# Optimization experiments

Measured on AMD Instinct MI355X. Metric: run time of the kernel, lower is better.

Reference implementation:

```python
import jax, jax.numpy as jnp
import numpy as np

N = 16384
IN_DIM = 11
D = 64
L = 4
K = 16 + 1  # self.k + 1 (n >= k+1)
EPS = 1e-5


def _bn(x, g, b):
    # BatchNorm1d in training mode: biased batch stats over the edge/node axis
    m = jnp.mean(x, axis=0)
    v = jnp.var(x, axis=0)
    return g * (x - m) * jax.lax.rsqrt(v + EPS) + b


def _mlp(x, W1, b1, g1, be1, W2, b2, g2, be2):
    x = jax.nn.relu(_bn(x @ W1 + b1, g1, be1))
    x = jax.nn.relu(_bn(x @ W2 + b2, g2, be2))
    return x


def _knn_edges(h):
    # torch.cdist + topk(-d, K); row 0 of idx.T is the (self) nearest node
    hs = jax.lax.stop_gradient(h)  # only indices are used downstream
    sq = jnp.sum(hs * hs, axis=-1)
    d2 = sq[:, None] + sq[None, :] - 2.0 * (hs @ hs.T)  # (n, n)
    d = jnp.sqrt(jnp.maximum(d2, 0.0))
    _, idx = jax.lax.top_k(-d, K)  # (n, K)
    frm = jnp.tile(idx[:, 0], K - 1)            # from_nodes = row0 repeated
    to = idx[:, 1:].T.reshape(-1)               # to_nodes = rows 1..K-1 flattened
    return frm, to


def setup_inputs() -> dict:
    key = jax.random.key(0)
    ks = jax.random.split(key, 8)
    s = 0.05
    inp = {
        "pos": jax.random.normal(ks[0], (N, IN_DIM), jnp.float32),
        "lin_in_W": jax.random.normal(ks[1], (IN_DIM, D), jnp.float32) * s,
        "lin_in_b": jnp.zeros((D,), jnp.float32),
        "pred_W": jax.random.normal(ks[2], (D, 1), jnp.float32) * s,
        "pred_b": jnp.zeros((1,), jnp.float32),
    }
    i = 3
    for pre in ("msg", "upd"):
        inp[f"{pre}_W1"] = jax.random.normal(ks[i], (L, 2 * D, D), jnp.float32) * s
        inp[f"{pre}_b1"] = jnp.zeros((L, D), jnp.float32)
        inp[f"{pre}_g1"] = jnp.ones((L, D), jnp.float32)
        inp[f"{pre}_be1"] = jnp.zeros((L, D), jnp.float32)
        inp[f"{pre}_W2"] = jax.random.normal(ks[i + 1], (L, D, D), jnp.float32) * s
        inp[f"{pre}_b2"] = jnp.zeros((L, D), jnp.float32)
        inp[f"{pre}_g2"] = jnp.ones((L, D), jnp.float32)
        inp[f"{pre}_be2"] = jnp.zeros((L, D), jnp.float32)
        i += 2
    return inp


def reference(pos, lin_in_W, lin_in_b, pred_W, pred_b,
              msg_W1, msg_b1, msg_g1, msg_be1, msg_W2, msg_b2, msg_g2, msg_be2,
              upd_W1, upd_b1, upd_g1, upd_be1, upd_W2, upd_b2, upd_g2, upd_be2):
    h = pos @ lin_in_W + lin_in_b  # (n, d)
    for l in range(L):
        frm, to = _knn_edges(h)
        # PyG source_to_target: h_j = h[edge_index[0]] (source), h_i = h[edge_index[1]] (dest)
        h_i = h[to]
        h_j = h[frm]
        msg = _mlp(jnp.concatenate([h_i, h_j], axis=-1),
                   msg_W1[l], msg_b1[l], msg_g1[l], msg_be1[l],
                   msg_W2[l], msg_b2[l], msg_g2[l], msg_be2[l])  # (e, d)
        agg = jax.ops.segment_sum(msg, to, num_segments=N)  # scatter-add at dest
        upd = _mlp(jnp.concatenate([h, agg], axis=-1),
                   upd_W1[l], upd_b1[l], upd_g1[l], upd_be1[l],
                   upd_W2[l], upd_b2[l], upd_g2[l], upd_be2[l])
        h = h + upd  # residual
    h_graph = jnp.mean(h, axis=0, keepdims=True)  # global_mean_pool, single graph
    out = h_graph @ pred_W + pred_b
    return out.reshape(-1)
```

## Files before the change

### kernel.cpp

```cpp
#include <hip/hip_runtime.h>

#define NN 16384
#define KP1 17
#define EE (NN*16)
#define CAP 448

typedef short bf16x8 __attribute__((ext_vector_type(8)));
typedef float f32x16 __attribute__((ext_vector_type(16)));

__device__ __forceinline__ ushort f2bf(float f) {
  unsigned u = __float_as_uint(f);
  unsigned r = (u + 0x7fffu + ((u >> 16) & 1u)) >> 16;
  return (ushort)r;
}
__device__ __forceinline__ float bf2f(ushort s) { return __uint_as_float(((unsigned)s) << 16); }

__global__ __launch_bounds__(256) void k_lin_in(const float* __restrict__ pos,
    const float* __restrict__ W, const float* __restrict__ b, float* __restrict__ h) {
  const int t = blockIdx.x*256 + threadIdx.x;
  const int n = t >> 6, c = t & 63;
  float acc = b[c];
  #pragma unroll
  for (int k = 0; k < 11; ++k) acc = fmaf(pos[n*11+k], W[k*64+c], acc);
  h[t] = acc;
}

__global__ __launch_bounds__(256) void k_prep_all(const float* __restrict__ h, float* __restrict__ sq,
    ushort* __restrict__ pk, ushort* __restrict__ hbh, ushort* __restrict__ hbl) {
  const int row = blockIdx.x*256 + threadIdx.x;
  const int tile = row >> 5, rl = row & 31;
  const float4* rp = (const float4*)(h + (size_t)row*64);
  float s = 0.f;
  #pragma unroll
  for (int q = 0; q < 16; ++q) {
    const float4 x = rp[q];
    s += x.x*x.x + x.y*x.y + x.z*x.z + x.w*x.w;
    ushort4 hi, lo;
    hi.x = f2bf(x.x); lo.x = f2bf(x.x - bf2f(hi.x));
    hi.y = f2bf(x.y); lo.y = f2bf(x.y - bf2f(hi.y));
    hi.z = f2bf(x.z); lo.z = f2bf(x.z - bf2f(hi.z));
    hi.w = f2bf(x.w); lo.w = f2bf(x.w - bf2f(hi.w));
    *(ushort4*)(hbh + (size_t)row*64 + q*4) = hi;
    *(ushort4*)(hbl + (size_t)row*64 + q*4) = lo;
    const int ks = q >> 2, sub = (q >> 1) & 1, e = (q & 1)*4;
    const int lane = rl + 32*sub;
    ushort* base = pk + (size_t)tile*4096 + ks*1024 + (size_t)lane*8 + e;
    *(ushort4*)(base)       = hi;
    *(ushort4*)(base + 512) = lo;
  }
  sq[row] = s;
}

__global__ __launch_bounds__(256) void k_wprep(const float* __restrict__ W1all,
    const float* __restrict__ W2all, ushort* __restrict__ wp1, ushort* __restrict__ wp2) {
  const int t = blockIdx.x*256 + threadIdx.x;
  if (t < 4096) {
    const int lane = t & 63, ks = (t>>6)&7, mt = (t>>9)&1, l = t>>10;
    const int m = mt*32 + (lane&31);
    const int k0 = ks*16 + (lane>>5)*8;
    const float* w = W1all + l*8192;
    ushort* dst = wp1 + ((((size_t)l*2 + mt)*8 + ks)*2)*512 + (size_t)lane*8;
    #pragma unroll
    for (int e = 0; e < 8; ++e) {
      const float v = w[(k0+e)*64 + m];
      const ushort hi = f2bf(v);
      dst[e] = hi; dst[512+e] = f2bf(v - bf2f(hi));
    }
  } else if (t < 6144) {
    const int t2 = t - 4096;
    const int lane = t2 & 63, ks = (t2>>6)&3, mt = (t2>>8)&1, l = t2>>9;
    const int m = mt*32 + (lane&31);
    const int k0 = ks*16 + (lane>>5)*8;
    const float* w = W2all + l*4096;
    ushort* dst = wp2 + ((((size_t)l*2 + mt)*4 + ks)*2)*512 + (size_t)lane*8;
    #pragma unroll
    for (int e = 0; e < 8; ++e) {
      const float v = w[(k0+e)*64 + m];
      const ushort hi = f2bf(v);
      dst[e] = hi; dst[512+e] = f2bf(v - bf2f(hi));
    }
  }
}

struct F8 { bf16x8 h0,h1,h2,h3,l0,l1,l2,l3; };

__device__ __forceinline__ void ldf(const ushort* __restrict__ pk, int tile, int lane, F8& f) {
  const ushort* tp = pk + (size_t)tile*4096 + (size_t)lane*8;
  f.h0 = *(const bf16x8*)(tp);
  f.l0 = *(const bf16x8*)(tp + 512);
  f.h1 = *(const bf16x8*)(tp + 1024);
  f.l1 = *(const bf16x8*)(tp + 1536);
  f.h2 = *(const bf16x8*)(tp + 2048);
  f.l2 = *(const bf16x8*)(tp + 2560);
  f.h3 = *(const bf16x8*)(tp + 3072);
  f.l3 = *(const bf16x8*)(tp + 3584);
}

#define MF(A,B,C) __builtin_amdgcn_mfma_f32_32x32x16_bf16(A,B,C,0,0,0)

__device__ __forceinline__ void tile_keys2(const F8& fa, const F8& fb,
    const bf16x8 (&bqh)[4], const bf16x8 (&bql)[4], const float* __restrict__ sq,
    const int ta, const int tb, const int lhi, float (&ka)[16], float (&kb)[16]) {
  f32x16 a, b;
  #pragma unroll
  for (int i = 0; i < 16; ++i) { a[i] = 0.f; b[i] = 0.f; }
  a = MF(fa.h0, bqh[0], a);  b = MF(fb.h0, bqh[0], b);
  a = MF(fa.h0, bql[0], a);  b = MF(fb.h0, bql[0], b);
  a = MF(fa.l0, bqh[0], a);  b = MF(fb.l0, bqh[0], b);
  a = MF(fa.h1, bqh[1], a);  b = MF(fb.h1, bqh[1], b);
  a = MF(fa.h1, bql[1], a);  b = MF(fb.h1, bql[1], b);
  a = MF(fa.l1, bqh[1], a);  b = MF(fb.l1, bqh[1], b);
  a = MF(fa.h2, bqh[2], a);  b = MF(fb.h2, bqh[2], b);
  a = MF(fa.h2, bql[2], a);  b = MF(fb.h2, bql[2], b);
  a = MF(fa.l2, bqh[2], a);  b = MF(fb.l2, bqh[2], b);
  a = MF(fa.h3, bqh[3], a);  b = MF(fb.h3, bqh[3], b);
  a = MF(fa.h3, bql[3], a);  b = MF(fb.h3, bql[3], b);
  a = MF(fa.l3, bqh[3], a);  b = MF(fb.l3, bqh[3], b);
  const int c0a = ta*32, c0b = tb*32;
  #pragma unroll
  for (int g = 0; g < 4; ++g) {
    const float4 va = *(const float4*)(sq + c0a + g*8 + 4*lhi);
    const float4 vb = *(const float4*)(sq + c0b + g*8 + 4*lhi);
    ka[g*4+0] = fmaf(-2.f, a[g*4+0], va.x);
    ka[g*4+1] = fmaf(-2.f, a[g*4+1], va.y);
    ka[g*4+2] = fmaf(-2.f, a[g*4+2], va.z);
    ka[g*4+3] = fmaf(-2.f, a[g*4+3], va.w);
    kb[g*4+0] = fmaf(-2.f, b[g*4+0], vb.x);
    kb[g*4+1] = fmaf(-2.f, b[g*4+1], vb.y);
    kb[g*4+2] = fmaf(-2.f, b[g*4+2], vb.z);
    kb[g*4+3] = fmaf(-2.f, b[g*4+3], vb.w);
  }
}

#define HIST1(K) { _Pragma("unroll") for (int r = 0; r < 16; ++r) { \
    unsigned x = __float_as_uint(K[r]); x = (x & 0x80000000u) ? ~x : (x | 0x80000000u); \
    atomicAdd(&hist[x >> 24][qcol], 1u); } }
#define HIST2(K) { _Pragma("unroll") for (int r = 0; r < 16; ++r) { \
    unsigned x = __float_as_uint(K[r]); x = (x & 0x80000000u) ? ~x : (x | 0x80000000u); \
    if ((x >> 24) == b1) atomicAdd(&hist[(x >> 16) & 255u][qcol], 1u); } }
#define COLLECT(K, TILE) { _Pragma("unroll") for (int r = 0; r < 16; ++r) { \
    if (K[r] <= bfq) { \
      unsigned x = __float_as_uint(K[r]); x = (x & 0x80000000u) ? ~x : (x | 0x80000000u); \
      const unsigned slot = atomicAdd(&ccnt[qcol], 1u); \
      if (slot < CAP) { \
        const int cidx = (TILE)*32 + (r & 3) + 8*(r >> 2) + 4*lhi; \
        coll[(size_t)q*CAP + slot] = ((unsigned long long)x << 32) | (unsigned)cidx; } } } }

__global__ __launch_bounds__(512) void k_knn(const ushort* __restrict__ pk,
    const float* __restrict__ sq, unsigned long long* __restrict__ coll,
    unsigned* __restrict__ gcnt) {
  __shared__ unsigned hist[256][32];
  __shared__ unsigned part[16][32];
  __shared__ unsigned bin1s[32], below1s[32];
  __shared__ float boundf[32];
  __shared__ unsigned ccnt[32];
  const int tid = threadIdx.x;
  const int wave = tid >> 6, lane = tid & 63;
  const int qcol = lane & 31, lhi = lane >> 5;
  const int qt = blockIdx.x;
  const int q = qt*32 + qcol;

  for (int i = tid; i < 256*32; i += 512) ((unsigned*)hist)[i] = 0u;
  if (tid < 32) ccnt[tid] = 0u;

  bf16x8 bqh[4], bql[4];
  {
    const ushort* tp = pk + (size_t)qt*4096 + (size_t)lane*8;
    #pragma unroll
    for (int ks = 0; ks < 4; ++ks) {
      bqh[ks] = *(const bf16x8*)(tp + ks*1024);
      bql[ks] = *(const bf16x8*)(tp + ks*1024 + 512);
    }
  }
  __syncthreads();

  #pragma unroll 1
  for (int s = 0; s < 8; s += 2) {
    F8 fa, fb;
    ldf(pk, wave*8 + s, lane, fa);
    ldf(pk, wave*8 + s + 1, lane, fb);
    float ka[16], kb[16];
    tile_keys2(fa, fb, bqh, bql, sq, wave*8 + s, wave*8 + s + 1, lhi, ka, kb);
    HIST1(ka)
    HIST1(kb)
  }
  __syncthreads();
  {
    const int qq = tid & 31, j = tid >> 5;
    unsigned ssum = 0;
    #pragma unroll
    for (int i = 0; i < 16; ++i) ssum += hist[j*16 + i][qq];
    part[j][qq] = ssum;
  }
  __syncthreads();
  if (tid < 32) {
    unsigned cum = 0;
    int jj = 0;
    while (jj < 15 && cum + part[jj][tid] < KP1) { cum += part[jj][tid]; ++jj; }
    unsigned c2 = cum, b = 0, fnd = 0;
    #pragma unroll 1
    for (int i = 0; i < 16; ++i) {
      const unsigned nc = c2 + hist[jj*16 + i][tid];
      if (!fnd && nc >= KP1) { b = (unsigned)(jj*16 + i); fnd = 1; break; }
      c2 = nc;
    }
    bin1s[tid] = b; below1s[tid] = c2;
  }
  __syncthreads();
  for (int i = tid; i < 256*32; i += 512) ((unsigned*)hist)[i] = 0u;
  __syncthreads();
  const unsigned b1 = bin1s[qcol];

  #pragma unroll 1
  for (int s = 0; s < 8; s += 2) {
    F8 fa, fb;
    ldf(pk, wave*8 + s, lane, fa);
    ldf(pk, wave*8 + s + 1, lane, fb);
    float ka[16], kb[16];
    tile_keys2(fa, fb, bqh, bql, sq, wave*8 + s, wave*8 + s + 1, lhi, ka, kb);
    HIST2(ka)
    HIST2(kb)
  }
  __syncthreads();
  {
    const int qq = tid & 31, j = tid >> 5;
    unsigned ssum = 0;
    #pragma unroll
    for (int i = 0; i < 16; ++i) ssum += hist[j*16 + i][qq];
    part[j][qq] = ssum;
  }
  __syncthreads();
  if (tid < 32) {
    unsigned cum = below1s[tid];
    int jj = 0;
    while (jj < 15 && cum + part[jj][tid] < KP1) { cum += part[jj][tid]; ++jj; }
    unsigned c2 = cum, b = 255u, fnd = 0;
    #pragma unroll 1
    for (int i = 0; i < 16; ++i) {
      c2 += hist[jj*16 + i][tid];
      if (!fnd && c2 >= KP1) { b = (unsigned)(jj*16 + i); fnd = 1; }
    }
    const unsigned bu = (bin1s[tid] << 24) | (b << 16) | 0xFFFFu;
    boundf[tid] = __uint_as_float((bu & 0x80000000u) ? (bu & 0x7fffffffu) : ~bu);
  }
  __syncthreads();
  const float bfq = boundf[qcol];

  #pragma unroll 1
  for (int s = 0; s < 64; s += 2) {
    F8 fa, fb;
    ldf(pk, wave*64 + s, lane, fa);
    ldf(pk, wave*64 + s + 1, lane, fb);
    float ka[16], kb[16];
    tile_keys2(fa, fb, bqh, bql, sq, wave*64 + s, wave*64 + s + 1, lhi, ka, kb);
    COLLECT(ka, wave*64 + s)
    COLLECT(kb, wave*64 + s + 1)
  }
  __syncthreads();
  if (tid < 32) gcnt[qt*32 + tid] = min(ccnt[tid], (unsigned)CAP);
}

__global__ __launch_bounds__(256) void k_select(const unsigned long long* __restrict__ coll,
    const unsigned* __restrict__ gcnt, int* __restrict__ idxout, unsigned* __restrict__ cnt) {
  const int gw = (blockIdx.x*256 + threadIdx.x) >> 6;
  const int lane = threadIdx.x & 63;
  const int m = min((int)gcnt[gw], CAP);
  const unsigned long long* cp = coll + (size_t)gw*CAP;
  unsigned long long a0,a1,a2,a3,a4,a5,a6;
  a0 = (lane       < m) ? cp[lane      ] : ~0ULL;
  a1 = (lane +  64 < m) ? cp[lane +  64] : ~0ULL;
  a2 = (lane + 128 < m) ? cp[lane + 128] : ~0ULL;
  a3 = (lane + 192 < m) ? cp[lane + 192] : ~0ULL;
  a4 = (lane + 256 < m) ? cp[lane + 256] : ~0ULL;
  a5 = (lane + 320 < m) ? cp[lane + 320] : ~0ULL;
  a6 = (lane + 384 < m) ? cp[lane + 384] : ~0ULL;
  #define CS(X,Y) { if (Y < X) { const unsigned long long t_ = X; X = Y; Y = t_; } }
  CS(a0,a1) CS(a2,a3) CS(a4,a5)
  CS(a1,a2) CS(a3,a4) CS(a5,a6)
  CS(a0,a1) CS(a2,a3) CS(a4,a5)
  CS(a1,a2) CS(a3,a4) CS(a5,a6)
  CS(a0,a1) CS(a2,a3) CS(a4,a5)
  CS(a1,a2) CS(a3,a4) CS(a5,a6)
  CS(a0,a1) CS(a2,a3) CS(a4,a5)
  #undef CS
  #pragma unroll
  for (int p = 0; p < KP1; ++p) {
    unsigned long long w = a0;
    #pragma unroll
    for (int d = 1; d < 64; d <<= 1) {
      const unsigned long long o = __shfl_xor(w, d);
      w = o < w ? o : w;
    }
    if (lane == 0) {
      const int ni = (int)(unsigned)(w & 0xffffffffULL);
      idxout[gw*KP1 + p] = ni;
      if (p > 0) atomicAdd(&cnt[ni], 1u);
    }
    if (a0 == w) { a0=a1; a1=a2; a2=a3; a3=a4; a4=a5; a5=a6; a6=~0ULL; }
  }
}

__global__ __launch_bounds__(256) void k_scan(const unsigned* __restrict__ cnt,
    unsigned* __restrict__ offs, unsigned* __restrict__ pos) {
  __shared__ unsigned ps[256];
  const int t = threadIdx.x;
  unsigned s = 0;
  #pragma unroll 4
  for (int j = 0; j < 64; ++j) s += cnt[t*64 + j];
  ps[t] = s;
  __syncthreads();
  for (int d = 1; d < 256; d <<= 1) {
    const unsigned v = (t >= d) ? ps[t-d] : 0u;
    __syncthreads();
    ps[t] += v;
    __syncthreads();
  }
  unsigned run = ps[t] - s;
  #pragma unroll 4
  for (int j = 0; j < 64; ++j) {
    const unsigned c = cnt[t*64 + j];
    offs[t*64 + j] = run; pos[t*64 + j] = run;
    run += c;
  }
}

__global__ __launch_bounds__(256) void k_scatter(const int* __restrict__ idx,
    unsigned* __restrict__ pos, unsigned* __restrict__ sortedE) {
  const int e = blockIdx.x*256 + threadIdx.x;
  const int i = e & (NN-1), k = e >> 14;
  const int to = idx[i*KP1 + k + 1];
  sortedE[atomicAdd(&pos[to], 1u)] = (unsigned)e;
}

__global__ __launch_bounds__(256) void k_agg(const ushort* __restrict__ y2,
    const unsigned* __restrict__ offs, const unsigned* __restrict__ cnt,
    const unsigned* __restrict__ sortedE,
    const float* __restrict__ s, const float* __restrict__ s2,
    const float* __restrict__ gam, const float* __restrict__ bet, float* __restrict__ agg) {
  __shared__ float scs[64], shs[64];
  const int tid = threadIdx.x;
  if (tid < 64) {
    const float m = s[tid] * (1.f/(float)EE);
    const float v = fmaxf(s2[tid]*(1.f/(float)EE) - m*m, 0.f);
    const float scv = gam[tid]*rsqrtf(v + 1e-5f);
    scs[tid] = scv; shs[tid] = bet[tid] - m*scv;
  }
  __syncthreads();
  const int t = blockIdx.x*256 + tid;
  const int n = t >> 4, c4 = t & 15;
  const unsigned o = offs[n], m = cnt[n];
  const float sc0 = scs[c4*4+0], sc1 = scs[c4*4+1], sc2 = scs[c4*4+2], sc3 = scs[c4*4+3];
  const float sh0 = shs[c4*4+0], sh1 = shs[c4*4+1], sh2 = shs[c4*4+2], sh3 = shs[c4*4+3];
  float a0=0.f, a1=0.f, a2=0.f, a3=0.f;
  for (unsigned j = 0; j < m; ++j) {
    const unsigned e = sortedE[o + j];
    const ushort4 v = *(const ushort4*)(y2 + (size_t)e*64 + c4*4);
    a0 += fmaxf(fmaf(bf2f(v.x), sc0, sh0), 0.f);
    a1 += fmaxf(fmaf(bf2f(v.y), sc1, sh1), 0.f);
    a2 += fmaxf(fmaf(bf2f(v.z), sc2, sh2), 0.f);
    a3 += fmaxf(fmaf(bf2f(v.w), sc3, sh3), 0.f);
  }
  *(float4*)(agg + (size_t)n*64 + c4*4) = make_float4(a0, a1, a2, a3);
}

__global__ __launch_bounds__(256) void k_eA(const ushort* __restrict__ hbh,
    const ushort* __restrict__ hbl, const int* __restrict__ idx,
    const ushort* __restrict__ wp1, const float* __restrict__ b1, ushort* __restrict__ y1) {
  __shared__ ushort wlds[16384];
  __shared__ float b1s[64];
  __shared__ ushort ytr[4][32][40];
  const int tid = threadIdx.x, wave = tid >> 6, lane = tid & 63;
  const int n = lane & 31, lhi = lane >> 5;
  for (int i = tid*8; i < 16384; i += 2048) *(uint4*)(wlds+i) = *(const uint4*)(wp1+i);
  if (tid < 64) b1s[tid] = b1[tid];
  __syncthreads();

  const int tile = blockIdx.x*4 + wave;
  const int e = tile*32 + n;
  const int i_ = e & (NN-1), kk = e >> 14;
  const int to = idx[i_*KP1 + kk + 1];
  const int fr = idx[i_*KP1];

  bf16x8 bh[8], bl[8];
  #pragma unroll
  for (int ks = 0; ks < 4; ++ks) {
    const size_t off = (size_t)to*64 + ks*16 + lhi*8;
    bh[ks] = *(const bf16x8*)(hbh + off);
    bl[ks] = *(const bf16x8*)(hbl + off);
  }
  #pragma unroll
  for (int ks = 0; ks < 4; ++ks) {
    const size_t off = (size_t)fr*64 + ks*16 + lhi*8;
    bh[4+ks] = *(const bf16x8*)(hbh + off);
    bl[4+ks] = *(const bf16x8*)(hbl + off);
  }

  f32x16 aA[2], aB[2];
  #pragma unroll
  for (int i = 0; i < 16; ++i) { aA[0][i]=0.f; aA[1][i]=0.f; aB[0][i]=0.f; aB[1][i]=0.f; }
  #pragma unroll
  for (int mt = 0; mt < 2; ++mt) {
    #pragma unroll
    for (int ks = 0; ks < 8; ++ks) {
      const ushort* wp = wlds + ((mt*8+ks)*2)*512 + lane*8;
      const bf16x8 wh = *(const bf16x8*)wp;
      const bf16x8 wl = *(const bf16x8*)(wp + 512);
      aA[mt] = MF(wh, bh[ks], aA[mt]);
      aB[mt] = MF(wh, bl[ks], aB[mt]);
      aB[mt] = MF(wl, bh[ks], aB[mt]);
    }
  }

  #pragma unroll
  for (int mt = 0; mt < 2; ++mt) {
    #pragma unroll
    for (int g = 0; g < 4; ++g) {
      const int mb = mt*32 + g*8 + lhi*4;
      ushort4 p;
      p.x = f2bf(aA[mt][g*4+0] + aB[mt][g*4+0] + b1s[mb+0]);
      p.y = f2bf(aA[mt][g*4+1] + aB[mt][g*4+1] + b1s[mb+1]);
      p.z = f2bf(aA[mt][g*4+2] + aB[mt][g*4+2] + b1s[mb+2]);
      p.w = f2bf(aA[mt][g*4+3] + aB[mt][g*4+3] + b1s[mb+3]);
      *(ushort4*)(&ytr[wave][n][g*8 + lhi*4]) = p;
    }
    __syncthreads();
    #pragma unroll
    for (int rep = 0; rep < 2; ++rep) {
      const int s = rep*256 + tid;
      const int w = s >> 7, inner = s & 127;
      const int nn = inner >> 2, c8 = inner & 3;
      const bf16x8 v = *(const bf16x8*)(&ytr[w][nn][c8*8]);
      const int tw = blockIdx.x*4 + w;
      *(bf16x8*)(y1 + ((size_t)tw*32 + nn)*64 + mt*32 + c8*8) = v;
    }
    __syncthreads();
  }
}

__global__ __launch_bounds__(256) void k_estats(const ushort* __restrict__ y,
    float* __restrict__ s, float* __restrict__ s2) {
  __shared__ float ls[16][64], lq[16][64];
  const int tid = threadIdx.x;
  const int c4 = tid & 15, g = tid >> 4;
  float a0=0,a1=0,a2=0,a3=0,b0=0,b1=0,b2=0,b3=0;
  for (int r = blockIdx.x*16 + g; r < EE; r += 4096) {
    const ushort4 v = *(const ushort4*)(y + (size_t)r*64 + c4*4);
    const float f0 = bf2f(v.x), f1 = bf2f(v.y), f2 = bf2f(v.z), f3 = bf2f(v.w);
    a0 += f0; b0 = fmaf(f0,f0,b0);
    a1 += f1; b1 = fmaf(f1,f1,b1);
    a2 += f2; b2 = fmaf(f2,f2,b2);
    a3 += f3; b3 = fmaf(f3,f3,b3);
  }
  ls[g][c4*4+0]=a0; ls[g][c4*4+1]=a1; ls[g][c4*4+2]=a2; ls[g][c4*4+3]=a3;
  lq[g][c4*4+0]=b0; lq[g][c4*4+1]=b1; lq[g][c4*4+2]=b2; lq[g][c4*4+3]=b3;
  __syncthreads();
  if (tid < 64) {
    float sa = 0.f, sb = 0.f;
    #pragma unroll
    for (int gg = 0; gg < 16; ++gg) { sa += ls[gg][tid]; sb += lq[gg][tid]; }
    atomicAdd(&s[tid], sa); atomicAdd(&s2[tid], sb);
  }
}

__global__ __launch_bounds__(256) void k_eB(const ushort* __restrict__ y1,
    const float* __restrict__ s, const float* __restrict__ s2,
    const float* __restrict__ gam, const float* __restrict__ bet,
    const ushort* __restrict__ wp2, const float* __restrict__ b2, ushort* __restrict__ y2) {
  __shared__ ushort wlds[8192];
  __shared__ float scs[64], shs[64], b2s[64];
  __shared__ ushort ytr[4][32][40];
  const int tid = threadIdx.x, wave = tid >> 6, lane = tid & 63;
  const int n = lane & 31, lhi = lane >> 5;
  for (int i = tid*8; i < 8192; i += 2048) *(uint4*)(wlds+i) = *(const uint4*)(wp2+i);
  if (tid < 64) {
    const float m = s[tid] * (1.f/(float)EE);
    const float v = fmaxf(s2[tid]*(1.f/(float)EE) - m*m, 0.f);
    const float scv = gam[tid]*rsqrtf(v + 1e-5f);
    scs[tid] = scv; shs[tid] = bet[tid] - m*scv; b2s[tid] = b2[tid];
  }
  __syncthreads();

  const int tile = blockIdx.x*4 + wave;
  const int e = tile*32 + n;

  bf16x8 bh[4], bl[4];
  #pragma unroll
  for (int ks = 0; ks < 4; ++ks) {
    const ushort4 v0 = *(const ushort4*)(y1 + (size_t)e*64 + ks*16 + lhi*8);
    const ushort4 v1 = *(const ushort4*)(y1 + (size_t)e*64 + ks*16 + lhi*8 + 4);
    const int k0 = ks*16 + lhi*8;
    float x[8];
    x[0]=bf2f(v0.x); x[1]=bf2f(v0.y); x[2]=bf2f(v0.z); x[3]=bf2f(v0.w);
    x[4]=bf2f(v1.x); x[5]=bf2f(v1.y); x[6]=bf2f(v1.z); x[7]=bf2f(v1.w);
    #pragma unroll
    for (int j = 0; j < 8; ++j) {
      const float f = fmaxf(fmaf(x[j], scs[k0+j], shs[k0+j]), 0.f);
      const ushort hi = f2bf(f);
      bh[ks][j] = (short)hi;
      bl[ks][j] = (short)f2bf(f - bf2f(hi));
    }
  }

  f32x16 aA[2], aB[2];
  #pragma unroll
  for (int i = 0; i < 16; ++i) { aA[0][i]=0.f; aA[1][i]=0.f; aB[0][i]=0.f; aB[1][i]=0.f; }
  #pragma unroll
  for (int mt = 0; mt < 2; ++mt) {
    #pragma unroll
    for (int ks = 0; ks < 4; ++ks) {
      const ushort* wp = wlds + ((mt*4+ks)*2)*512 + lane*8;
      const bf16x8 wh = *(const bf16x8*)wp;
      const bf16x8 wl = *(const bf16x8*)(wp + 512);
      aA[mt] = MF(wh, bh[ks], aA[mt]);
      aB[mt] = MF(wh, bl[ks], aB[mt]);
      aB[mt] = MF(wl, bh[ks], aB[mt]);
    }
  }

  #pragma unroll
  for (int mt = 0; mt < 2; ++mt) {
    #pragma unroll
    for (int g = 0; g < 4; ++g) {
      const int mb = mt*32 + g*8 + lhi*4;
      ushort4 p;
      p.x = f2bf(aA[mt][g*4+0] + aB[mt][g*4+0] + b2s[mb+0]);
      p.y = f2bf(aA[mt][g*4+1] + aB[mt][g*4+1] + b2s[mb+1]);
      p.z = f2bf(aA[mt][g*4+2] + aB[mt][g*4+2] + b2s[mb+2]);
      p.w = f2bf(aA[mt][g*4+3] + aB[mt][g*4+3] + b2s[mb+3]);
      *(ushort4*)(&ytr[wave][n][g*8 + lhi*4]) = p;
    }
    __syncthreads();
    #pragma unroll
    for (int rep = 0; rep < 2; ++rep) {
      const int ss = rep*256 + tid;
      const int w = ss >> 7, inner = ss & 127;
      const int nn = inner >> 2, c8 = inner & 3;
      const bf16x8 v = *(const bf16x8*)(&ytr[w][nn][c8*8]);
      const int tw = blockIdx.x*4 + w;
      *(bf16x8*)(y2 + ((size_t)tw*32 + nn)*64 + mt*32 + c8*8) = v;
    }
    __syncthreads();
  }
}

__global__ __launch_bounds__(256) void k_colstats(const float* __restrict__ x, const int rows,
    float* __restrict__ s, float* __restrict__ s2) {
  __shared__ float ls[4][64], ls2[4][64];
  const int tid = threadIdx.x;
  const int c = tid & 63, g = tid >> 6;
  float a = 0.f, b = 0.f;
  for (int r = blockIdx.x*4 + g; r < rows; r += 1024) {
    const float v = x[(size_t)r*64 + c];
    a += v; b = fmaf(v, v, b);
  }
  ls[g][c] = a; ls2[g][c] = b;
  __syncthreads();
  if (tid < 64) {
    atomicAdd(&s[tid],  ls[0][tid]+ls[1][tid]+ls[2][tid]+ls[3][tid]);
    atomicAdd(&s2[tid], ls2[0][tid]+ls2[1][tid]+ls2[2][tid]+ls2[3][tid]);
  }
}

__device__ __forceinline__ void fmarow(float (&acc)[64], const float (*ws)[64], int kk, float xv) {
  #pragma unroll
  for (int cq = 0; cq < 16; ++cq) {
    const float4 w4 = *(const float4*)&ws[kk][cq*4];
    acc[cq*4]   = fmaf(xv, w4.x, acc[cq*4]);
    acc[cq*4+1] = fmaf(xv, w4.y, acc[cq*4+1]);
    acc[cq*4+2] = fmaf(xv, w4.z, acc[cq*4+2]);
    acc[cq*4+3] = fmaf(xv, w4.w, acc[cq*4+3]);
  }
}

__global__ __launch_bounds__(256) void k_mlpA_cat(const float* __restrict__ h,
    const float* __restrict__ agg, const float* __restrict__ W1, const float* __restrict__ b1,
    float* __restrict__ y) {
  __shared__ __align__(16) float ws[128][64];
  const int tid = threadIdx.x;
  for (int t = tid; t < 128*64/4; t += 256) ((float4*)ws)[t] = ((const float4*)W1)[t];
  __syncthreads();
  const int n = blockIdx.x*256 + tid;
  float acc[64];
  #pragma unroll
  for (int c = 0; c < 64; ++c) acc[c] = b1[c];
  const float4* xa = (const float4*)(h + (size_t)n*64);
  #pragma unroll 2
  for (int kb = 0; kb < 16; ++kb) {
    const float4 x4 = xa[kb];
    fmarow(acc, ws, kb*4,   x4.x); fmarow(acc, ws, kb*4+1, x4.y);
    fmarow(acc, ws, kb*4+2, x4.z); fmarow(acc, ws, kb*4+3, x4.w);
  }
  const float4* xb = (const float4*)(agg + (size_t)n*64);
  #pragma unroll 2
  for (int kb = 0; kb < 16; ++kb) {
    const float4 x4 = xb[kb];
    fmarow(acc, ws, 64+kb*4,   x4.x); fmarow(acc, ws, 64+kb*4+1, x4.y);
    fmarow(acc, ws, 64+kb*4+2, x4.z); fmarow(acc, ws, 64+kb*4+3, x4.w);
  }
  float4* yo = (float4*)(y + (size_t)n*64);
  #pragma unroll
  for (int q = 0; q < 16; ++q) yo[q] = make_float4(acc[4*q], acc[4*q+1], acc[4*q+2], acc[4*q+3]);
}

__global__ __launch_bounds__(256) void k_mlpB(float* __restrict__ y,
    const float* __restrict__ s, const float* __restrict__ s2,
    const float* __restrict__ g, const float* __restrict__ be,
    const float* __restrict__ W2, const float* __restrict__ b2, const float invR) {
  __shared__ __align__(16) float ws[64][64];
  __shared__ float sc[64], sh[64];
  const int tid = threadIdx.x;
  for (int t = tid; t < 64*64/4; t += 256) ((float4*)ws)[t] = ((const float4*)W2)[t];
  if (tid < 64) {
    const float m = s[tid]*invR;
    const float v = fmaxf(s2[tid]*invR - m*m, 0.f);
    const float scv = g[tid]*rsqrtf(v + 1e-5f);
    sc[tid] = scv; sh[tid] = be[tid] - m*scv;
  }
  __syncthreads();
  const int e = blockIdx.x*256 + tid;
  float acc[64];
  #pragma unroll
  for (int c = 0; c < 64; ++c) acc[c] = b2[c];
  const float4* yr = (const float4*)(y + (size_t)e*64);
  #pragma unroll 2
  for (int kb = 0; kb < 16; ++kb) {
    const float4 x4 = yr[kb];
    const int k0 = kb*4;
    fmarow(acc, ws, k0,   fmaxf(fmaf(x4.x, sc[k0],   sh[k0]),   0.f));
    fmarow(acc, ws, k0+1, fmaxf(fmaf(x4.y, sc[k0+1], sh[k0+1]), 0.f));
    fmarow(acc, ws, k0+2, fmaxf(fmaf(x4.z, sc[k0+2], sh[k0+2]), 0.f));
    fmarow(acc, ws, k0+3, fmaxf(fmaf(x4.w, sc[k0+3], sh[k0+3]), 0.f));
  }
  float4* yo = (float4*)(y + (size_t)e*64);
  #pragma unroll
  for (int q = 0; q < 16; ++q) yo[q] = make_float4(acc[4*q], acc[4*q+1], acc[4*q+2], acc[4*q+3]);
}

__global__ __launch_bounds__(256) void k_updC(const float* __restrict__ y,
    const float* __restrict__ s, const float* __restrict__ s2,
    const float* __restrict__ g, const float* __restrict__ be,
    float* __restrict__ h, const float invR) {
  __shared__ float sc[64], sh[64];
  const int tid = threadIdx.x;
  if (tid < 64) {
    const float m = s[tid]*invR;
    const float v = fmaxf(s2[tid]*invR - m*m, 0.f);
    const float scv = g[tid]*rsqrtf(v + 1e-5f);
    sc[tid] = scv; sh[tid] = be[tid] - m*scv;
  }
  __syncthreads();
  const int t = blockIdx.x*256 + tid;
  const int c = t & 63;
  h[t] += fmaxf(fmaf(y[t], sc[c], sh[c]), 0.f);
}

__global__ void k_final(const float* __restrict__ hsum, const float* __restrict__ pW,
                        const float* __restrict__ pb, float* __restrict__ out) {
  const int c = threadIdx.x;
  float v = hsum[c] * (1.f/(float)NN) * pW[c];
  #pragma unroll
  for (int m = 32; m >= 1; m >>= 1) v += __shfl_xor(v, m, 64);
  if (c == 0) out[0] = v + pb[0];
}

extern "C" void kernel_launch(void* const* d_in, const int* in_sizes, int n_in,
                              void* d_out, int out_size, void* d_ws, size_t ws_size,
                              hipStream_t stream) {
  const float* pos   = (const float*)d_in[0];
  const float* linW  = (const float*)d_in[1];
  const float* linb  = (const float*)d_in[2];
  const float* predW = (const float*)d_in[3];
  const float* predb = (const float*)d_in[4];
  const float* mW1 = (const float*)d_in[5];
  const float* mb1 = (const float*)d_in[6];
  const float* mg1 = (const float*)d_in[7];
  const float* mbe1= (const float*)d_in[8];
  const float* mW2 = (const float*)d_in[9];
  const float* mb2 = (const float*)d_in[10];
  const float* mg2 = (const float*)d_in[11];
  const float* mbe2= (const float*)d_in[12];
  const float* uW1 = (const float*)d_in[13];
  const float* ub1 = (const float*)d_in[14];
  const float* ug1 = (const float*)d_in[15];
  const float* ube1= (const float*)d_in[16];
  const float* uW2 = (const float*)d_in[17];
  const float* ub2 = (const float*)d_in[18];
  const float* ug2 = (const float*)d_in[19];
  const float* ube2= (const float*)d_in[20];

  float* h     = (float*)d_ws;
  float* sq    = h + (size_t)NN*64;
  float* agg   = sq + NN;
  float* ubuf  = agg + (size_t)NN*64;
  float* stats = ubuf + (size_t)NN*64;
  int*   idx   = (int*)(stats + 640);
  char*  yb    = (char*)(idx + (size_t)NN*KP1);
  ushort* pk = (ushort*)yb;
  unsigned long long* coll = (unsigned long long*)(yb + 4194304);
  ushort* hbh = (ushort*)(yb + 62914560);
  ushort* hbl = hbh + (size_t)NN*64;
  ushort* y1 = (ushort*)yb;
  ushort* y2 = y1 + (size_t)EE*64;
  ushort* wp1 = (ushort*)(yb + 67108864);
  ushort* wp2 = wp1 + 4*16384;
  unsigned* cnt     = (unsigned*)ubuf;
  unsigned* offs    = cnt + NN;
  unsigned* pcur    = offs + NN;
  unsigned* sortedE = pcur + NN;
  unsigned* gcnt    = sortedE + EE;

  k_lin_in<<<NN*64/256, 256, 0, stream>>>(pos, linW, linb, h);
  k_wprep<<<24, 256, 0, stream>>>(mW1, mW2, wp1, wp2);
  for (int l = 0; l < 4; ++l) {
    k_prep_all<<<NN/256, 256, 0, stream>>>(h, sq, pk, hbh, hbl);
    k_knn<<<NN/32, 512, 0, stream>>>(pk, sq, coll, gcnt);
    hipMemsetAsync(cnt, 0, NN*sizeof(unsigned), stream);
    k_select<<<NN/4, 256, 0, stream>>>(coll, gcnt, idx, cnt);
    hipMemsetAsync(stats, 0, 640*sizeof(float), stream);
    k_scan<<<1, 256, 0, stream>>>(cnt, offs, pcur);
    k_scatter<<<EE/256, 256, 0, stream>>>(idx, pcur, sortedE);
    k_eA<<<EE/32/4, 256, 0, stream>>>(hbh, hbl, idx, wp1 + (size_t)l*16384, mb1 + l*64, y1);
    k_estats<<<256, 256, 0, stream>>>(y1, stats, stats+64);
    k_eB<<<EE/32/4, 256, 0, stream>>>(y1, stats, stats+64, mg1 + l*64, mbe1 + l*64,
                                      wp2 + (size_t)l*8192, mb2 + l*64, y2);
    k_estats<<<256, 256, 0, stream>>>(y2, stats+128, stats+192);
    k_agg<<<NN*16/256, 256, 0, stream>>>(y2, offs, cnt, sortedE, stats+128, stats+192,
                                         mg2 + l*64, mbe2 + l*64, agg);
    k_mlpA_cat<<<NN/256, 256, 0, stream>>>(h, agg, uW1 + l*8192, ub1 + l*64, ubuf);
    k_colstats<<<256, 256, 0, stream>>>(ubuf, NN, stats+256, stats+320);
    k_mlpB<<<NN/256, 256, 0, stream>>>(ubuf, stats+256, stats+320, ug1 + l*64, ube1 + l*64,
                                       uW2 + l*4096, ub2 + l*64, 1.f/(float)NN);
    k_colstats<<<256, 256, 0, stream>>>(ubuf, NN, stats+384, stats+448);
    k_updC<<<NN*64/256, 256, 0, stream>>>(ubuf, stats+384, stats+448, ug2 + l*64, ube2 + l*64,
                                          h, 1.f/(float)NN);
  }
  hipMemsetAsync(stats+512, 0, 128*sizeof(float), stream);
  k_colstats<<<256, 256, 0, stream>>>(h, NN, stats+512, stats+576);
  k_final<<<1, 64, 0, stream>>>(stats+512, predW, predb, (float*)d_out);
}
```

Measured before the change: 2.222 ms.

## Software-pipeline kNN tile loads and fuse residual update with next-layer prep

The kNN kernel's three passes now prefetch the next pair of bf16 tiles while MFMA results for the current pair are turned into histogram or collect updates, so load latency overlaps with compute. Key computation is folded directly into the histogram/collect macros instead of going through intermediate arrays. Separately, the residual update kernel for layers 0-2 is fused with the next layer's prep (squared norms, bf16 hi/lo split, packed tile layout), removing one kernel launch and one re-read of h per layer. Holding four tiles of fragments raises register pressure, which may lower occupancy. The fused kernel uses one thread per row, so its memory accesses are strided rather than coalesced.

Result: slower. 2.451 ms (+10.3%).

```diff
diff --git a/kernel.cpp b/kernel.cpp
--- a/kernel.cpp
+++ b/kernel.cpp
@@ -98,53 +98,47 @@
 
 #define MF(A,B,C) __builtin_amdgcn_mfma_f32_32x32x16_bf16(A,B,C,0,0,0)
 
-__device__ __forceinline__ void tile_keys2(const F8& fa, const F8& fb,
-    const bf16x8 (&bqh)[4], const bf16x8 (&bql)[4], const float* __restrict__ sq,
-    const int ta, const int tb, const int lhi, float (&ka)[16], float (&kb)[16]) {
-  f32x16 a, b;
-  #pragma unroll
-  for (int i = 0; i < 16; ++i) { a[i] = 0.f; b[i] = 0.f; }
-  a = MF(fa.h0, bqh[0], a);  b = MF(fb.h0, bqh[0], b);
-  a = MF(fa.h0, bql[0], a);  b = MF(fb.h0, bql[0], b);
-  a = MF(fa.l0, bqh[0], a);  b = MF(fb.l0, bqh[0], b);
-  a = MF(fa.h1, bqh[1], a);  b = MF(fb.h1, bqh[1], b);
-  a = MF(fa.h1, bql[1], a);  b = MF(fb.h1, bql[1], b);
-  a = MF(fa.l1, bqh[1], a);  b = MF(fb.l1, bqh[1], b);
-  a = MF(fa.h2, bqh[2], a);  b = MF(fb.h2, bqh[2], b);
-  a = MF(fa.h2, bql[2], a);  b = MF(fb.h2, bql[2], b);
-  a = MF(fa.l2, bqh[2], a);  b = MF(fb.l2, bqh[2], b);
-  a = MF(fa.h3, bqh[3], a);  b = MF(fb.h3, bqh[3], b);
-  a = MF(fa.h3, bql[3], a);  b = MF(fb.h3, bql[3], b);
-  a = MF(fa.l3, bqh[3], a);  b = MF(fb.l3, bqh[3], b);
-  const int c0a = ta*32, c0b = tb*32;
-  #pragma unroll
-  for (int g = 0; g < 4; ++g) {
-    const float4 va = *(const float4*)(sq + c0a + g*8 + 4*lhi);
-    const float4 vb = *(const float4*)(sq + c0b + g*8 + 4*lhi);
-    ka[g*4+0] = fmaf(-2.f, a[g*4+0], va.x);
-    ka[g*4+1] = fmaf(-2.f, a[g*4+1], va.y);
-    ka[g*4+2] = fmaf(-2.f, a[g*4+2], va.z);
-    ka[g*4+3] = fmaf(-2.f, a[g*4+3], va.w);
-    kb[g*4+0] = fmaf(-2.f, b[g*4+0], vb.x);
-    kb[g*4+1] = fmaf(-2.f, b[g*4+1], vb.y);
-    kb[g*4+2] = fmaf(-2.f, b[g*4+2], vb.z);
-    kb[g*4+3] = fmaf(-2.f, b[g*4+3], vb.w);
-  }
-}
-
-#define HIST1(K) { _Pragma("unroll") for (int r = 0; r < 16; ++r) { \
-    unsigned x = __float_as_uint(K[r]); x = (x & 0x80000000u) ? ~x : (x | 0x80000000u); \
-    atomicAdd(&hist[x >> 24][qcol], 1u); } }
-#define HIST2(K) { _Pragma("unroll") for (int r = 0; r < 16; ++r) { \
-    unsigned x = __float_as_uint(K[r]); x = (x & 0x80000000u) ? ~x : (x | 0x80000000u); \
-    if ((x >> 24) == b1) atomicAdd(&hist[(x >> 16) & 255u][qcol], 1u); } }
-#define COLLECT(K, TILE) { _Pragma("unroll") for (int r = 0; r < 16; ++r) { \
-    if (K[r] <= bfq) { \
-      unsigned x = __float_as_uint(K[r]); x = (x & 0x80000000u) ? ~x : (x | 0x80000000u); \
-      const unsigned slot = atomicAdd(&ccnt[qcol], 1u); \
-      if (slot < CAP) { \
-        const int cidx = (TILE)*32 + (r & 3) + 8*(r >> 2) + 4*lhi; \
-        coll[(size_t)q*CAP + slot] = ((unsigned long long)x << 32) | (unsigned)cidx; } } } }
+#define CHAIN2(FA, FB, A, B) { \
+  _Pragma("unroll") for (int i_ = 0; i_ < 16; ++i_) { A[i_] = 0.f; B[i_] = 0.f; } \
+  A = MF(FA.h0, bqh[0], A);  B = MF(FB.h0, bqh[0], B); \
+  A = MF(FA.h0, bql[0], A);  B = MF(FB.h0, bql[0], B); \
+  A = MF(FA.l0, bqh[0], A);  B = MF(FB.l0, bqh[0], B); \
+  A = MF(FA.h1, bqh[1], A);  B = MF(FB.h1, bqh[1], B); \
+  A = MF(FA.h1, bql[1], A);  B = MF(FB.h1, bql[1], B); \
+  A = MF(FA.l1, bqh[1], A);  B = MF(FB.l1, bqh[1], B); \
+  A = MF(FA.h2, bqh[2], A);  B = MF(FB.h2, bqh[2], B); \
+  A = MF(FA.h2, bql[2], A);  B = MF(FB.h2, bql[2], B); \
+  A = MF(FA.l2, bqh[2], A);  B = MF(FB.l2, bqh[2], B); \
+  A = MF(FA.h3, bqh[3], A);  B = MF(FB.h3, bqh[3], B); \
+  A = MF(FA.h3, bql[3], A);  B = MF(FB.h3, bql[3], B); \
+  A = MF(FA.l3, bqh[3], A);  B = MF(FB.l3, bqh[3], B); }
+
+#define HIST1_ACC(A, TILE) { const int c0_ = (TILE)*32; \
+  _Pragma("unroll") for (int g_ = 0; g_ < 4; ++g_) { \
+    const float4 v_ = *(const float4*)(sq + c0_ + g_*8 + 4*lhi); \
+    _Pragma("unroll") for (int j_ = 0; j_ < 4; ++j_) { \
+      const float key_ = fmaf(-2.f, A[g_*4+j_], (&v_.x)[j_]); \
+      unsigned x_ = __float_as_uint(key_); x_ = (x_ & 0x80000000u) ? ~x_ : (x_ | 0x80000000u); \
+      atomicAdd(&hist[x_ >> 24][qcol], 1u); } } }
+#define HIST2_ACC(A, TILE) { const int c0_ = (TILE)*32; \
+  _Pragma("unroll") for (int g_ = 0; g_ < 4; ++g_) { \
+    const float4 v_ = *(const float4*)(sq + c0_ + g_*8 + 4*lhi); \
+    _Pragma("unroll") for (int j_ = 0; j_ < 4; ++j_) { \
+      const float key_ = fmaf(-2.f, A[g_*4+j_], (&v_.x)[j_]); \
+      unsigned x_ = __float_as_uint(key_); x_ = (x_ & 0x80000000u) ? ~x_ : (x_ | 0x80000000u); \
+      if ((x_ >> 24) == b1) atomicAdd(&hist[(x_ >> 16) & 255u][qcol], 1u); } } }
+#define COLLECT_ACC(A, TILE) { const int c0_ = (TILE)*32; \
+  _Pragma("unroll") for (int g_ = 0; g_ < 4; ++g_) { \
+    const float4 v_ = *(const float4*)(sq + c0_ + g_*8 + 4*lhi); \
+    _Pragma("unroll") for (int j_ = 0; j_ < 4; ++j_) { \
+      const float key_ = fmaf(-2.f, A[g_*4+j_], (&v_.x)[j_]); \
+      if (key_ <= bfq) { \
+        unsigned x_ = __float_as_uint(key_); x_ = (x_ & 0x80000000u) ? ~x_ : (x_ | 0x80000000u); \
+        const unsigned slot_ = atomicAdd(&ccnt[qcol], 1u); \
+        if (slot_ < CAP) { \
+          const int r_ = g_*4 + j_; \
+          const int cidx_ = (TILE)*32 + (r_ & 3) + 8*(r_ >> 2) + 4*lhi; \
+          coll[(size_t)q*CAP + slot_] = ((unsigned long long)x_ << 32) | (unsigned)cidx_; } } } } }
 
 __global__ __launch_bounds__(512) void k_knn(const ushort* __restrict__ pk,
     const float* __restrict__ sq, unsigned long long* __restrict__ coll,
@@ -174,15 +168,24 @@
   }
   __syncthreads();
 
+  F8 fa, fb, fc, fd;
+
+  ldf(pk, wave*8, lane, fa);
+  ldf(pk, wave*8 + 1, lane, fb);
   #pragma unroll 1
-  for (int s = 0; s < 8; s += 2) {
-    F8 fa, fb;
-    ldf(pk, wave*8 + s, lane, fa);
-    ldf(pk, wave*8 + s + 1, lane, fb);
-    float ka[16], kb[16];
-    tile_keys2(fa, fb, bqh, bql, sq, wave*8 + s, wave*8 + s + 1, lhi, ka, kb);
-    HIST1(ka)
-    HIST1(kb)
+  for (int s = 0; s < 8; s += 4) {
+    const int t0 = wave*8 + s;
+    f32x16 a, b;
+    CHAIN2(fa, fb, a, b)
+    ldf(pk, t0 + 2, lane, fc);
+    ldf(pk, t0 + 3, lane, fd);
+    HIST1_ACC(a, t0)
+    HIST1_ACC(b, t0 + 1)
+    f32x16 c2, d2;
+    CHAIN2(fc, fd, c2, d2)
+    if (s + 4 < 8) { ldf(pk, t0 + 4, lane, fa); ldf(pk, t0 + 5, lane, fb); }
+    HIST1_ACC(c2, t0 + 2)
+    HIST1_ACC(d2, t0 + 3)
   }
   __syncthreads();
   {
@@ -211,15 +214,22 @@
   __syncthreads();
   const unsigned b1 = bin1s[qcol];
 
+  ldf(pk, wave*8, lane, fa);
+  ldf(pk, wave*8 + 1, lane, fb);
   #pragma unroll 1
-  for (int s = 0; s < 8; s += 2) {
-    F8 fa, fb;
-    ldf(pk, wave*8 + s, lane, fa);
-    ldf(pk, wave*8 + s + 1, lane, fb);
-    float ka[16], kb[16];
-    tile_keys2(fa, fb, bqh, bql, sq, wave*8 + s, wave*8 + s + 1, lhi, ka, kb);
-    HIST2(ka)
-    HIST2(kb)
+  for (int s = 0; s < 8; s += 4) {
+    const int t0 = wave*8 + s;
+    f32x16 a, b;
+    CHAIN2(fa, fb, a, b)
+    ldf(pk, t0 + 2, lane, fc);
+    ldf(pk, t0 + 3, lane, fd);
+    HIST2_ACC(a, t0)
+    HIST2_ACC(b, t0 + 1)
+    f32x16 c2, d2;
+    CHAIN2(fc, fd, c2, d2)
+    if (s + 4 < 8) { ldf(pk, t0 + 4, lane, fa); ldf(pk, t0 + 5, lane, fb); }
+    HIST2_ACC(c2, t0 + 2)
+    HIST2_ACC(d2, t0 + 3)
   }
   __syncthreads();
   {
@@ -246,15 +256,22 @@
   __syncthreads();
   const float bfq = boundf[qcol];
 
+  ldf(pk, wave*64, lane, fa);
+  ldf(pk, wave*64 + 1, lane, fb);
   #pragma unroll 1
-  for (int s = 0; s < 64; s += 2) {
-    F8 fa, fb;
-    ldf(pk, wave*64 + s, lane, fa);
-    ldf(pk, wave*64 + s + 1, lane, fb);
-    float ka[16], kb[16];
-    tile_keys2(fa, fb, bqh, bql, sq, wave*64 + s, wave*64 + s + 1, lhi, ka, kb);
-    COLLECT(ka, wave*64 + s)
-    COLLECT(kb, wave*64 + s + 1)
+  for (int s = 0; s < 64; s += 4) {
+    const int t0 = wave*64 + s;
+    f32x16 a, b;
+    CHAIN2(fa, fb, a, b)
+    ldf(pk, t0 + 2, lane, fc);
+    ldf(pk, t0 + 3, lane, fd);
+    COLLECT_ACC(a, t0)
+    COLLECT_ACC(b, t0 + 1)
+    f32x16 c2, d2;
+    CHAIN2(fc, fd, c2, d2)
+    if (s + 4 < 64) { ldf(pk, t0 + 4, lane, fa); ldf(pk, t0 + 5, lane, fb); }
+    COLLECT_ACC(c2, t0 + 2)
+    COLLECT_ACC(d2, t0 + 3)
   }
   __syncthreads();
   if (tid < 32) gcnt[qt*32 + tid] = min(ccnt[tid], (unsigned)CAP);
@@ -652,6 +669,53 @@
   const int t = blockIdx.x*256 + tid;
   const int c = t & 63;
   h[t] += fmaxf(fmaf(y[t], sc[c], sh[c]), 0.f);
+}
+
+__global__ __launch_bounds__(256) void k_updC_prep(const float* __restrict__ y,
+    const float* __restrict__ s, const float* __restrict__ s2,
+    const float* __restrict__ g, const float* __restrict__ be,
+    float* __restrict__ h, const float invR,
+    float* __restrict__ sq, ushort* __restrict__ pk,
+    ushort* __restrict__ hbh, ushort* __restrict__ hbl) {
+  __shared__ float sc[64], sh[64];
+  const int tid = threadIdx.x;
+  if (tid < 64) {
+    const float m = s[tid]*invR;
+    const float v = fmaxf(s2[tid]*invR - m*m, 0.f);
+    const float scv = g[tid]*rsqrtf(v + 1e-5f);
+    sc[tid] = scv; sh[tid] = be[tid] - m*scv;
+  }
+  __syncthreads();
+  const int row = blockIdx.x*256 + tid;
+  const int tile = row >> 5, rl = row & 31;
+  float4* hp = (float4*)(h + (size_t)row*64);
+  const float4* yp = (const float4*)(y + (size_t)row*64);
+  float ssum = 0.f;
+  #pragma unroll
+  for (int q = 0; q < 16; ++q) {
+    const float4 yv = yp[q];
+    float4 x = hp[q];
+    const int k0 = q*4;
+    x.x += fmaxf(fmaf(yv.x, sc[k0+0], sh[k0+0]), 0.f);
+    x.y += fmaxf(fmaf(yv.y, sc[k0+1], sh[k0+1]), 0.f);
+    x.z += fmaxf(fmaf(yv.z, sc[k0+2], sh[k0+2]), 0.f);
+    x.w += fmaxf(fmaf(yv.w, sc[k0+3], sh[k0+3]), 0.f);
+    hp[q] = x;
+    ssum += x.x*x.x + x.y*x.y + x.z*x.z + x.w*x.w;
+    ushort4 hi, lo;
+    hi.x = f2bf(x.x); lo.x = f2bf(x.x - bf2f(hi.x));
+    hi.y = f2bf(x.y); lo.y = f2bf(x.y - bf2f(hi.y));
+    hi.z = f2bf(x.z); lo.z = f2bf(x.z - bf2f(hi.z));
+    hi.w = f2bf(x.w); lo.w = f2bf(x.w - bf2f(hi.w));
+    *(ushort4*)(hbh + (size_t)row*64 + q*4) = hi;
+    *(ushort4*)(hbl + (size_t)row*64 + q*4) = lo;
+    const int ks = q >> 2, sub = (q >> 1) & 1, e = (q & 1)*4;
+    const int lane = rl + 32*sub;
+    ushort* base = pk + (size_t)tile*4096 + ks*1024 + (size_t)lane*8 + e;
+    *(ushort4*)(base)       = hi;
+    *(ushort4*)(base + 512) = lo;
+  }
+  sq[row] = ssum;
 }
 
 __global__ void k_final(const float* __restrict__ hsum, const float* __restrict__ pW,
@@ -711,8 +775,8 @@
 
   k_lin_in<<<NN*64/256, 256, 0, stream>>>(pos, linW, linb, h);
   k_wprep<<<24, 256, 0, stream>>>(mW1, mW2, wp1, wp2);
+  k_prep_all<<<NN/256, 256, 0, stream>>>(h, sq, pk, hbh, hbl);
   for (int l = 0; l < 4; ++l) {
-    k_prep_all<<<NN/256, 256, 0, stream>>>(h, sq, pk, hbh, hbl);
     k_knn<<<NN/32, 512, 0, stream>>>(pk, sq, coll, gcnt);
     hipMemsetAsync(cnt, 0, NN*sizeof(unsigned), stream);
     k_select<<<NN/4, 256, 0, stream>>>(coll, gcnt, idx, cnt);
@@ -731,8 +795,13 @@
     k_mlpB<<<NN/256, 256, 0, stream>>>(ubuf, stats+256, stats+320, ug1 + l*64, ube1 + l*64,
                                        uW2 + l*4096, ub2 + l*64, 1.f/(float)NN);
     k_colstats<<<256, 256, 0, stream>>>(ubuf, NN, stats+384, stats+448);
-    k_updC<<<NN*64/256, 256, 0, stream>>>(ubuf, stats+384, stats+448, ug2 + l*64, ube2 + l*64,
-                                          h, 1.f/(float)NN);
+    if (l < 3) {
+      k_updC_prep<<<NN/256, 256, 0, stream>>>(ubuf, stats+384, stats+448, ug2 + l*64, ube2 + l*64,
+                                              h, 1.f/(float)NN, sq, pk, hbh, hbl);
+    } else {
+      k_updC<<<NN*64/256, 256, 0, stream>>>(ubuf, stats+384, stats+448, ug2 + l*64, ube2 + l*64,
+                                            h, 1.f/(float)NN);
+    }
   }
   hipMemsetAsync(stats+512, 0, 128*sizeof(float), stream);
   k_colstats<<<256, 256, 0, stream>>>(h, NN, stats+512, stats+576);
```
